# Performance work log

Measured on AMD Instinct MI355X. Metric: run time of the kernel, lower is better.

## Reference

```python
import jax, jax.numpy as jnp
import numpy as np

N_NODES = 30000
N_EDGES = 300000
NUM_GRAPHS = 512
HID = 600
IN_FEATS = 9
NUM_TASKS = 128


def setup_inputs() -> dict:
    key = jax.random.key(0)
    ks = jax.random.split(key, 20)
    s = 0.05  # small init scale to keep activations bounded over 5 layers
    inp = {
        'x': jax.random.normal(ks[0], (N_NODES, IN_FEATS), jnp.float32),
        'edge_index': jax.random.randint(ks[1], (2, N_EDGES), 0, N_NODES, jnp.int64),
        'batch_ind': jnp.sort(jax.random.randint(ks[2], (N_NODES,), 0, NUM_GRAPHS, jnp.int64)),
        'w1_0': jax.random.normal(ks[3], (IN_FEATS, HID), jnp.float32) * s,
        'b1_0': jax.random.normal(ks[4], (HID,), jnp.float32) * s,
        'w2_0': jax.random.normal(ks[5], (HID, HID), jnp.float32) * s,
        'b2_0': jax.random.normal(ks[6], (HID,), jnp.float32) * s,
        'w1_r': jax.random.normal(ks[7], (4, HID, HID), jnp.float32) * s,
        'b1_r': jax.random.normal(ks[8], (4, HID), jnp.float32) * s,
        'w2_r': jax.random.normal(ks[9], (4, HID, HID), jnp.float32) * s,
        'b2_r': jax.random.normal(ks[10], (4, HID), jnp.float32) * s,
        'cw1': jax.random.normal(ks[11], (HID, 256), jnp.float32) * s,
        'cb1': jax.random.normal(ks[12], (256,), jnp.float32) * s,
        'cw2': jax.random.normal(ks[13], (256, 256), jnp.float32) * s,
        'cb2': jax.random.normal(ks[14], (256,), jnp.float32) * s,
        'cw3': jax.random.normal(ks[15], (256, NUM_TASKS), jnp.float32) * s,
        'cb3': jax.random.normal(ks[16], (NUM_TASKS,), jnp.float32) * s,
    }
    return inp


def _gin_conv(h, edge_index, w1, b1, w2, b2):
    # sum-aggregate neighbor features: messages flow src -> dst
    msgs = h[edge_index[0]]                                   # [E, d] gather
    agg = jax.ops.segment_sum(msgs, edge_index[1], num_segments=N_NODES)
    z = h + agg                                               # (1 + eps) * x + agg, eps = 0
    z = jax.nn.relu(z @ w1 + b1) @ w2 + b2                    # per-layer MLP [in, 600, 600]
    return z


def _forward(x, edge_index, batch_ind, w1_0, b1_0, w2_0, b2_0,
             w1_r, b1_r, w2_r, b2_r, cw1, cb1, cw2, cb2, cw3, cb3):
    h = _gin_conv(x, edge_index, w1_0, b1_0, w2_0, b2_0)
    h = jax.nn.relu(h)  # inter-layer activation (dropout is identity in eval)
    for i in range(4):  # layers 1..4 (fixed, structurally distinct params)
        h = _gin_conv(h, edge_index, w1_r[i], b1_r[i], w2_r[i], b2_r[i])
        if i < 3:
            h = jax.nn.relu(h)  # no act/dropout after final GNN layer (jk=None)
    feats = jax.ops.segment_sum(h, batch_ind, num_segments=NUM_GRAPHS)  # global_add_pool
    z = jax.nn.relu(feats @ cw1 + cb1)
    z = jax.nn.relu(z @ cw2 + cb2)
    return z @ cw3 + cb3  # [NUM_GRAPHS, NUM_TASKS]


def reference(x, edge_index, batch_ind, w1_0, b1_0, w2_0, b2_0,
              w1_r, b1_r, w2_r, b2_r, cw1, cb1, cw2, cb2, cw3, cb3):
    return _forward(x, edge_index, batch_ind, w1_0, b1_0, w2_0, b2_0,
                    w1_r, b1_r, w2_r, b2_r, cw1, cb1, cw2, cb2, cw3, cb3)
```

## Files before the change

kernel.cpp:

```cpp
#include <hip/hip_runtime.h>

#define N_NODES 30000
#define N_EDGES 300000
#define NUM_GRAPHS 512
#define HID 600
#define IN_FEATS 9
#define NUM_TASKS 128

#define MPAD 30208
#define HPAD 640
#define K0PAD 32

typedef __attribute__((ext_vector_type(4))) float f32x4;
typedef __attribute__((ext_vector_type(8))) short bf16x8;


__device__ __forceinline__ float bflo(unsigned int v) {
  union { unsigned int u; float f; } c; c.u = v << 16; return c.f;
}
__device__ __forceinline__ float bfhi(unsigned int v) {
  union { unsigned int u; float f; } c; c.u = v & 0xffff0000u; return c.f;
}
__device__ __forceinline__ unsigned short f2bf(float f) {
  union { float f; unsigned int u; } c; c.f = f;
  unsigned int u = c.u;
  return (unsigned short)((u + 0x7fffu + ((u >> 16) & 1u)) >> 16);
}
__device__ __forceinline__ unsigned int pack2(float a, float b) {
  return (unsigned int)f2bf(a) | ((unsigned int)f2bf(b) << 16);
}


__global__ void k_setup(const float* __restrict__ w1_0,
                        const float* __restrict__ b1_0, const float* __restrict__ b2_0,
                        const float* __restrict__ b1_r, const float* __restrict__ b2_r,
                        const float* __restrict__ x,
                        const int* __restrict__ e_dst, const int* __restrict__ batch,
                        unsigned short* __restrict__ wt0, float* __restrict__ biases,
                        unsigned short* __restrict__ xb,
                        int* __restrict__ counts, int* __restrict__ gcnt) {
  const int S0 = HPAD * K0PAD;
  const int S1 = 10 * HPAD;
  const int S2 = MPAD * K0PAD;
  const int S3 = N_EDGES;
  int idx = blockIdx.x * 256 + threadIdx.x;
  if (idx < S0) {
    int n = idx / K0PAD, k = idx % K0PAD;
    float v = (n < HID && k < IN_FEATS) ? w1_0[(size_t)k * HID + n] : 0.f;
    wt0[idx] = f2bf(v);
    return;
  }
  idx -= S0;
  if (idx < S1) {
    int w = idx / HPAD, i = idx % HPAD;
    float v = 0.f;
    if (i < HID) {
      if (w == 0) v = b1_0[i];
      else if (w == 1) v = b2_0[i];
      else if (w < 6) v = b1_r[(size_t)(w - 2) * HID + i];
      else v = b2_r[(size_t)(w - 6) * HID + i];
    }
    biases[idx] = v;
    return;
  }
  idx -= S1;
  if (idx < S2) {
    int m = idx >> 5, k = idx & 31;
    float v = (m < N_NODES && k < IN_FEATS) ? x[(size_t)m * IN_FEATS + k] : 0.f;
    xb[idx] = f2bf(v);
    return;
  }
  idx -= S2;
  if (idx < S3) {
    atomicAdd(&counts[e_dst[idx]], 1);
    return;
  }
  idx -= S3;
  if (idx < N_NODES) {
    atomicAdd(&gcnt[batch[idx]], 1);
  }
}


__global__ __launch_bounds__(1024) void k_exscan(const int* __restrict__ in,
                                                 int* __restrict__ out,
                                                 int* cursor, int n) {
  __shared__ int buf[1024];
  int tid = threadIdx.x;
  int CH = (n + 1023) / 1024;
  int base = tid * CH;
  int s = 0;
  for (int j = 0; j < CH; ++j) {
    int i = base + j;
    if (i < n) s += in[i];
  }
  buf[tid] = s;
  __syncthreads();
  for (int off = 1; off < 1024; off <<= 1) {
    int t = (tid >= off) ? buf[tid - off] : 0;
    __syncthreads();
    buf[tid] += t;
    __syncthreads();
  }
  int pre = (tid == 0) ? 0 : buf[tid - 1];
  for (int j = 0; j < CH; ++j) {
    int i = base + j;
    if (i <= n) out[i] = pre;
    if (i < n) {
      int v = in[i];
      if (cursor) cursor[i] = pre;
      pre += v;
    }
  }
}

__global__ __launch_bounds__(256) void k_scan1(const int* __restrict__ in,
                                               int* __restrict__ partials, int n) {
  __shared__ int buf[256];
  int i = blockIdx.x * 256 + threadIdx.x;
  buf[threadIdx.x] = (i < n) ? in[i] : 0;
  __syncthreads();
  for (int off = 128; off; off >>= 1) {
    if (threadIdx.x < off) buf[threadIdx.x] += buf[threadIdx.x + off];
    __syncthreads();
  }
  if (threadIdx.x == 0) partials[blockIdx.x] = buf[0];
}

__global__ __launch_bounds__(256) void k_scan3(const int* __restrict__ in,
                                               const int* __restrict__ poff,
                                               int* __restrict__ out,
                                               int* __restrict__ cursor, int n) {
  __shared__ int buf[256];
  int b = blockIdx.x, t = threadIdx.x;
  int i = b * 256 + t;
  int v = (i < n) ? in[i] : 0;
  buf[t] = v;
  __syncthreads();
  for (int off = 1; off < 256; off <<= 1) {
    int x = (t >= off) ? buf[t - off] : 0;
    __syncthreads();
    buf[t] += x;
    __syncthreads();
  }
  int base = poff[b];
  int excl = base + buf[t] - v;
  if (i < n) {
    out[i] = excl;
    cursor[i] = excl;
    if (i == n - 1) out[n] = base + buf[t];
  }
}

__global__ void k_scatter(const int* __restrict__ src, const int* __restrict__ dst,
                          int* __restrict__ cursor, int* __restrict__ edge_src, int E) {
  int e = blockIdx.x * blockDim.x + threadIdx.x;
  if (e < E) {
    int pos = atomicAdd(&cursor[dst[e]], 1);
    edge_src[pos] = src[e];
  }
}


__global__ __launch_bounds__(256) void k_wt_tiled(
    const float* __restrict__ w2_0, const float* __restrict__ w1_r,
    const float* __restrict__ w2_r, unsigned short* __restrict__ wts) {
  __shared__ float tile[64][65];
  int b = blockIdx.x;
  int w = b / 100;
  int tb = b % 100;
  int tn = (tb % 10) * 64;
  int tk = (tb / 10) * 64;
  const float* W;
  if (w == 0) W = w2_0;
  else if (w < 5) W = w1_r + (size_t)(w - 1) * HID * HID;
  else W = w2_r + (size_t)(w - 5) * HID * HID;
  int t = threadIdx.x;
  int lx = t & 63, ly = t >> 6;
#pragma unroll
  for (int i = 0; i < 16; ++i) {
    int k = tk + ly + i * 4;
    int n = tn + lx;
    float v = (k < HID && n < HID) ? W[(size_t)k * HID + n] : 0.f;
    tile[ly + i * 4][lx] = v;
  }
  __syncthreads();
  unsigned short* dst = wts + (size_t)w * HPAD * HPAD;
#pragma unroll
  for (int i = 0; i < 16; ++i) {
    int n = tn + ly + i * 4;
    int k = tk + lx;
    dst[(size_t)n * HPAD + k] = f2bf(tile[lx][ly + i * 4]);
  }
}


template <int U>
__global__ __launch_bounds__(256) void k_agg_bf16(
    const unsigned int* __restrict__ h, const int* __restrict__ ptr,
    const int* __restrict__ esrc, unsigned int* __restrict__ z, int n_nodes) {
  int wave = threadIdx.x >> 6, lane = threadIdx.x & 63;
  int node = blockIdx.x * 4 + wave;
  if (node >= n_nodes) return;
  int beg = ptr[node], end = ptr[node + 1];
  const unsigned int* hn = h + (size_t)node * U;
  float a0[5], a1[5];
#pragma unroll
  for (int i = 0; i < 5; ++i) {
    int u = lane + i * 64;
    if (u < U) { unsigned int v = hn[u]; a0[i] = bflo(v); a1[i] = bfhi(v); }
    else { a0[i] = 0.f; a1[i] = 0.f; }
  }
  int e = beg;
  for (; e + 4 <= end; e += 4) {
    const unsigned int* p0 = h + (size_t)esrc[e] * U;
    const unsigned int* p1 = h + (size_t)esrc[e + 1] * U;
    const unsigned int* p2 = h + (size_t)esrc[e + 2] * U;
    const unsigned int* p3 = h + (size_t)esrc[e + 3] * U;
    unsigned int v0[5], v1[5], v2[5], v3[5];
#pragma unroll
    for (int i = 0; i < 5; ++i) {
      int u = lane + i * 64;
      if (u < U) { v0[i] = p0[u]; v1[i] = p1[u]; v2[i] = p2[u]; v3[i] = p3[u]; }
      else { v0[i] = 0; v1[i] = 0; v2[i] = 0; v3[i] = 0; }
    }
#pragma unroll
    for (int i = 0; i < 5; ++i) {
      a0[i] += (bflo(v0[i]) + bflo(v1[i])) + (bflo(v2[i]) + bflo(v3[i]));
      a1[i] += (bfhi(v0[i]) + bfhi(v1[i])) + (bfhi(v2[i]) + bfhi(v3[i]));
    }
  }
  for (; e < end; ++e) {
    const unsigned int* p0 = h + (size_t)esrc[e] * U;
#pragma unroll
    for (int i = 0; i < 5; ++i) {
      int u = lane + i * 64;
      if (u < U) { unsigned int v = p0[u]; a0[i] += bflo(v); a1[i] += bfhi(v); }
    }
  }
  unsigned int* zn = z + (size_t)node * U;
#pragma unroll
  for (int i = 0; i < 5; ++i) {
    int u = lane + i * 64;
    if (u < U) zn[u] = pack2(a0[i], a1[i]);
  }
}


#define GLOAD(gptr, lptr)                                                            \
  __builtin_amdgcn_global_load_lds(                                                  \
      (const __attribute__((address_space(1))) unsigned int*)(gptr),                 \
      (__attribute__((address_space(3))) unsigned int*)(lptr), 16, 0, 0)

template <int SWZ>
__global__ __launch_bounds__(512, 6) void k_mgemm_t(
    const unsigned short* __restrict__ A, const unsigned short* __restrict__ Bt,
    const float* __restrict__ bias, unsigned short* __restrict__ C,
    int lda, int ldb, int ldc, int K, int relu, int gy) {
  int G = gridDim.x;
  int orig = blockIdx.x;
  int q = G >> 3, r = G & 7;
  int xcd = orig & 7, local = orig >> 3;
  int wgid = (xcd < r ? xcd * (q + 1) : r * (q + 1) + (xcd - r) * q) + local;
  int n0 = (wgid % gy) * 128;
  int m0 = (wgid / gy) * 128;

  __shared__ unsigned short smem[3 * 4096 * 2];
  unsigned short* Asb = smem;
  unsigned short* Bsb = smem + 12288;

  int t = threadIdx.x;
  int lane = t & 63, wave = t >> 6;
  int wm = (wave >> 2) * 64;
  int wn = (wave & 3) * 32;

  f32x4 acc[4][2] = {};

  int off = t * 8;
  int rm = off >> 5, rk = off & 31;
  int rksrc = SWZ ? ((((rk >> 3) ^ (rm & 3)) & 3) << 3) : rk;

  const unsigned short* Ar = A + (size_t)(m0 + rm) * lda + rksrc;
  const unsigned short* Br = Bt + (size_t)(n0 + rm) * ldb + rksrc;

  int nt = K >> 5;
  GLOAD(Ar, Asb + off);
  GLOAD(Br, Bsb + off);
  if (nt > 1) {
    GLOAD(Ar + 32, Asb + 4096 + off);
    GLOAD(Br + 32, Bsb + 4096 + off);
  }

  int qq = lane >> 4;
  int ra = wm + (lane & 15);
  int rb = wn + (lane & 15);
  int kka = SWZ ? ((qq ^ (ra & 3)) << 3) : (qq << 3);
  int kkb = SWZ ? ((qq ^ (rb & 3)) << 3) : (qq << 3);
  int cur = 0;

  for (int tt = 0; tt < nt; ++tt) {
    if (tt + 1 < nt) {
      asm volatile("s_waitcnt vmcnt(2)" ::: "memory");
    } else {
      asm volatile("s_waitcnt vmcnt(0)" ::: "memory");
    }
    __builtin_amdgcn_s_barrier();
    if (tt + 2 < nt) {
      int k2 = (tt + 2) << 5;
      int nb = cur + 2; if (nb >= 3) nb -= 3;
      GLOAD(Ar + k2, Asb + nb * 4096 + off);
      GLOAD(Br + k2, Bsb + nb * 4096 + off);
    }
    bf16x8 a[4], b[2];
#pragma unroll
    for (int i = 0; i < 4; ++i)
      a[i] = *(const bf16x8*)(Asb + cur * 4096 + (ra + i * 16) * 32 + kka);
#pragma unroll
    for (int j = 0; j < 2; ++j)
      b[j] = *(const bf16x8*)(Bsb + cur * 4096 + (rb + j * 16) * 32 + kkb);
#pragma unroll
    for (int i = 0; i < 4; ++i)
#pragma unroll
      for (int j = 0; j < 2; ++j)
        acc[i][j] = __builtin_amdgcn_mfma_f32_16x16x32_bf16(b[j], a[i], acc[i][j], 0, 0, 0);
    cur += 1; if (cur >= 3) cur = 0;
  }

  __syncthreads();
  int colm = lane & 15;
  int nq = (lane >> 4) * 4;
#pragma unroll
  for (int j = 0; j < 2; ++j) {
    int nloc = wn + j * 16 + nq;
    f32x4 bv = *(const f32x4*)&bias[n0 + nloc];
#pragma unroll
    for (int i = 0; i < 4; ++i) {
      int mloc = wm + i * 16 + colm;
      float v0 = acc[i][j][0] + bv[0];
      float v1 = acc[i][j][1] + bv[1];
      float v2 = acc[i][j][2] + bv[2];
      float v3 = acc[i][j][3] + bv[3];
      if (relu) {
        v0 = fmaxf(v0, 0.f); v1 = fmaxf(v1, 0.f);
        v2 = fmaxf(v2, 0.f); v3 = fmaxf(v3, 0.f);
      }
      uint2 w;
      w.x = pack2(v0, v1);
      w.y = pack2(v2, v3);
      int nblk = (nloc >> 2) ^ ((mloc & 7) << 2);
      *(uint2*)&smem[mloc * 128 + nblk * 4] = w;
    }
  }
  __syncthreads();
#pragma unroll
  for (int p = 0; p < 4; ++p) {
    int idx = p * 4096 + t * 8;
    int mloc = idx >> 7;
    int ncol = idx & 127;
    int s = (mloc & 7) << 2;
    int nb0 = (ncol >> 2) ^ s;
    int nb1 = ((ncol >> 2) + 1) ^ s;
    uint2 w0 = *(uint2*)&smem[mloc * 128 + nb0 * 4];
    uint2 w1 = *(uint2*)&smem[mloc * 128 + nb1 * 4];
    uint4 w;
    w.x = w0.x; w.y = w0.y; w.z = w1.x; w.w = w1.y;
    *(uint4*)&C[(size_t)(m0 + mloc) * ldc + n0 + ncol] = w;
  }
}


__global__ __launch_bounds__(256) void k_poolcls(
    const unsigned int* __restrict__ h, const int* __restrict__ gptr,
    const float* __restrict__ cw1, const float* __restrict__ cb1,
    const float* __restrict__ cw2, const float* __restrict__ cb2,
    const float* __restrict__ cw3, const float* __restrict__ cb3,
    float* __restrict__ out) {
  const int U = HPAD / 2;
  __shared__ float red[4][HPAD];
  __shared__ float f[HPAD];
  __shared__ float red2[4][256];
  __shared__ float z1[256];
  __shared__ float z2[256];
  int g = blockIdx.x;
  int t = threadIdx.x;
  int wave = t >> 6, lane = t & 63;
  int beg = gptr[g], end = gptr[g + 1];

  {
    float a0[5] = {0.f, 0.f, 0.f, 0.f, 0.f}, a1[5] = {0.f, 0.f, 0.f, 0.f, 0.f};
    for (int i = beg + wave; i < end; i += 4) {
      const unsigned int* hi = h + (size_t)i * U;
#pragma unroll
      for (int j = 0; j < 5; ++j) {
        unsigned int v = hi[lane + j * 64];
        a0[j] += bflo(v); a1[j] += bfhi(v);
      }
    }
#pragma unroll
    for (int j = 0; j < 5; ++j) {
      int u = lane + j * 64;
      red[wave][2 * u] = a0[j];
      red[wave][2 * u + 1] = a1[j];
    }
  }
  __syncthreads();
  for (int c = t; c < HPAD; c += 256)
    f[c] = red[0][c] + red[1][c] + red[2][c] + red[3][c];
  __syncthreads();

  {
    float acc[4] = {0.f, 0.f, 0.f, 0.f};
    int k0 = wave * 150, k1 = k0 + 150;
    for (int k = k0; k < k1; ++k) {
      float fv = f[k];
      const float* row = cw1 + (size_t)k * 256;
#pragma unroll
      for (int j = 0; j < 4; ++j) acc[j] += fv * row[lane + j * 64];
    }
#pragma unroll
    for (int j = 0; j < 4; ++j) red2[wave][lane + j * 64] = acc[j];
  }
  __syncthreads();
  z1[t] = fmaxf(red2[0][t] + red2[1][t] + red2[2][t] + red2[3][t] + cb1[t], 0.f);
  __syncthreads();

  {
    float acc[4] = {0.f, 0.f, 0.f, 0.f};
    int k0 = wave * 64, k1 = k0 + 64;
    for (int k = k0; k < k1; ++k) {
      float zv = z1[k];
      const float* row = cw2 + (size_t)k * 256;
#pragma unroll
      for (int j = 0; j < 4; ++j) acc[j] += zv * row[lane + j * 64];
    }
    __syncthreads();
#pragma unroll
    for (int j = 0; j < 4; ++j) red2[wave][lane + j * 64] = acc[j];
  }
  __syncthreads();
  z2[t] = fmaxf(red2[0][t] + red2[1][t] + red2[2][t] + red2[3][t] + cb2[t], 0.f);
  __syncthreads();

  {
    float a0 = 0.f, a1 = 0.f;
    int k0 = wave * 64, k1 = k0 + 64;
    for (int k = k0; k < k1; ++k) {
      float zv = z2[k];
      const float* row = cw3 + (size_t)k * NUM_TASKS;
      a0 += zv * row[lane];
      a1 += zv * row[lane + 64];
    }
    __syncthreads();
    red2[wave][lane] = a0;
    red2[wave][lane + 64] = a1;
  }
  __syncthreads();
  if (t < NUM_TASKS)
    out[(size_t)g * NUM_TASKS + t] = red2[0][t] + red2[1][t] + red2[2][t] + red2[3][t] + cb3[t];
}


extern "C" void kernel_launch(void* const* d_in, const int* in_sizes, int n_in,
                              void* d_out, int out_size, void* d_ws, size_t ws_size,
                              hipStream_t stream) {
  const float* x      = (const float*)d_in[0];
  const int*   ei     = (const int*)d_in[1];
  const int*   batch  = (const int*)d_in[2];
  const float* w1_0   = (const float*)d_in[3];
  const float* b1_0   = (const float*)d_in[4];
  const float* w2_0   = (const float*)d_in[5];
  const float* b2_0   = (const float*)d_in[6];
  const float* w1_r   = (const float*)d_in[7];
  const float* b1_r   = (const float*)d_in[8];
  const float* w2_r   = (const float*)d_in[9];
  const float* b2_r   = (const float*)d_in[10];
  const float* cw1    = (const float*)d_in[11];
  const float* cb1    = (const float*)d_in[12];
  const float* cw2    = (const float*)d_in[13];
  const float* cb2    = (const float*)d_in[14];
  const float* cw3    = (const float*)d_in[15];
  const float* cb3    = (const float*)d_in[16];
  float* out = (float*)d_out;

  const int* e_src = ei;
  const int* e_dst = ei + N_EDGES;

  const size_t HBUF = (size_t)MPAD * HPAD;
  const size_t ZBUF = (size_t)MPAD * K0PAD;
  const size_t WT   = (size_t)HPAD * HPAD;
  const int NB = (N_NODES + 255) / 256;

  unsigned short* hA  = (unsigned short*)d_ws;
  unsigned short* hB  = hA + HBUF;
  unsigned short* hC  = hB + HBUF;
  unsigned short* z0  = hC + HBUF;
  unsigned short* xb  = z0 + ZBUF;
  unsigned short* wt0 = xb + ZBUF;
  unsigned short* wts = wt0 + (size_t)HPAD * K0PAD;
  float* biases = (float*)(wts + 9 * WT);
  int* row_ptr  = (int*)(biases + 10 * HPAD);
  int* counts   = row_ptr + (N_NODES + 1);
  int* edge_src = counts + N_NODES;
  int* gptr     = edge_src + N_EDGES;
  int* gcnt     = gptr + (NUM_GRAPHS + 1);
  int* partials = gcnt + NUM_GRAPHS;
  int* poff     = partials + (NB + 1);

  hipMemsetAsync(counts, 0, N_NODES * sizeof(int), stream);
  hipMemsetAsync(gcnt, 0, NUM_GRAPHS * sizeof(int), stream);
  {
    int total = HPAD * K0PAD + 10 * HPAD + MPAD * K0PAD + N_EDGES + N_NODES;
    k_setup<<<(total + 255) / 256, 256, 0, stream>>>(
        w1_0, b1_0, b2_0, b1_r, b2_r, x, e_dst, batch, wt0, biases, xb, counts, gcnt);
  }
  k_wt_tiled<<<9 * 100, 256, 0, stream>>>(w2_0, w1_r, w2_r, wts);

  k_scan1<<<NB, 256, 0, stream>>>(counts, partials, N_NODES);
  k_exscan<<<1, 1024, 0, stream>>>(partials, poff, nullptr, NB);
  k_scan3<<<NB, 256, 0, stream>>>(counts, poff, row_ptr, counts, N_NODES);
  k_scatter<<<(N_EDGES + 255) / 256, 256, 0, stream>>>(e_src, e_dst, counts, edge_src, N_EDGES);
  k_exscan<<<1, 1024, 0, stream>>>(gcnt, gptr, nullptr, NUM_GRAPHS);

  const int G16 = (MPAD / 128) * (HPAD / 128);
  const int GY = HPAD / 128;

  k_agg_bf16<K0PAD / 2><<<(N_NODES + 3) / 4, 256, 0, stream>>>(
      (const unsigned int*)xb, row_ptr, edge_src, (unsigned int*)z0, N_NODES);
  k_mgemm_t<0><<<G16, 512, 0, stream>>>(z0, wt0, biases + 0 * HPAD, hC, K0PAD, K0PAD, HPAD, K0PAD, 1, GY);
  k_mgemm_t<0><<<G16, 512, 0, stream>>>(hC, wts, biases + 1 * HPAD, hA, HPAD, HPAD, HPAD, HPAD, 1, GY);

  unsigned short* h = hA;
  unsigned short* z = hB;
  unsigned short* tb = hC;
  for (int i = 0; i < 4; ++i) {
    k_agg_bf16<HPAD / 2><<<(N_NODES + 3) / 4, 256, 0, stream>>>(
        (const unsigned int*)h, row_ptr, edge_src, (unsigned int*)z, N_NODES);
    if (i < 2) {
      k_mgemm_t<0><<<G16, 512, 0, stream>>>(z, wts + (1 + (size_t)i) * WT, biases + (2 + i) * HPAD, tb,
                                            HPAD, HPAD, HPAD, HPAD, 1, GY);
      k_mgemm_t<0><<<G16, 512, 0, stream>>>(tb, wts + (5 + (size_t)i) * WT, biases + (6 + i) * HPAD, z,
                                            HPAD, HPAD, HPAD, HPAD, 1, GY);
    } else {
      k_mgemm_t<1><<<G16, 512, 0, stream>>>(z, wts + (1 + (size_t)i) * WT, biases + (2 + i) * HPAD, tb,
                                            HPAD, HPAD, HPAD, HPAD, 1, GY);
      k_mgemm_t<1><<<G16, 512, 0, stream>>>(tb, wts + (5 + (size_t)i) * WT, biases + (6 + i) * HPAD, z,
                                            HPAD, HPAD, HPAD, HPAD, (i < 3) ? 1 : 0, GY);
    }
    unsigned short* tmp = h; h = z; z = tmp;
  }

  k_poolcls<<<NUM_GRAPHS, 256, 0, stream>>>((const unsigned int*)h, gptr,
                                            cw1, cb1, cw2, cb2, cw3, cb3, out);
}
```

Measured before the change: 709.9 us.

## Add full-width 128x640 GEMM tile kernel for last two GIN layers

Adds a wide GEMM kernel in which each block computes a 128-row by full 640-column output tile, so every A row-tile is loaded once and reused across all output columns. Each wave holds a 64x160 fp32 accumulator block, and the epilogue writes bf16 directly instead of staging through shared memory. The swizzled template variant is removed, and the plain kernel keeps the unswizzled path. Only the layer 3 and 4 MLP GEMMs use the wide kernel. The trade is much higher register and LDS use (launch bounds 512,2, three stages of 48KB), fewer blocks (236) and therefore lower occupancy, and uncoalesced 8-byte direct stores.

```diff
diff --git a/kernel.cpp b/kernel.cpp
--- a/kernel.cpp
+++ b/kernel.cpp
@@ -252,8 +252,7 @@
       (const __attribute__((address_space(1))) unsigned int*)(gptr),                 \
       (__attribute__((address_space(3))) unsigned int*)(lptr), 16, 0, 0)
 
-template <int SWZ>
-__global__ __launch_bounds__(512, 6) void k_mgemm_t(
+__global__ __launch_bounds__(512, 6) void k_mgemm(
     const unsigned short* __restrict__ A, const unsigned short* __restrict__ Bt,
     const float* __restrict__ bias, unsigned short* __restrict__ C,
     int lda, int ldb, int ldc, int K, int relu, int gy) {
@@ -278,10 +277,9 @@
 
   int off = t * 8;
   int rm = off >> 5, rk = off & 31;
-  int rksrc = SWZ ? ((((rk >> 3) ^ (rm & 3)) & 3) << 3) : rk;
-
-  const unsigned short* Ar = A + (size_t)(m0 + rm) * lda + rksrc;
-  const unsigned short* Br = Bt + (size_t)(n0 + rm) * ldb + rksrc;
+
+  const unsigned short* Ar = A + (size_t)(m0 + rm) * lda + rk;
+  const unsigned short* Br = Bt + (size_t)(n0 + rm) * ldb + rk;
 
   int nt = K >> 5;
   GLOAD(Ar, Asb + off);
@@ -291,11 +289,9 @@
     GLOAD(Br + 32, Bsb + 4096 + off);
   }
 
-  int qq = lane >> 4;
+  int kk = (lane >> 4) * 8;
   int ra = wm + (lane & 15);
   int rb = wn + (lane & 15);
-  int kka = SWZ ? ((qq ^ (ra & 3)) << 3) : (qq << 3);
-  int kkb = SWZ ? ((qq ^ (rb & 3)) << 3) : (qq << 3);
   int cur = 0;
 
   for (int tt = 0; tt < nt; ++tt) {
@@ -314,10 +310,10 @@
     bf16x8 a[4], b[2];
 #pragma unroll
     for (int i = 0; i < 4; ++i)
-      a[i] = *(const bf16x8*)(Asb + cur * 4096 + (ra + i * 16) * 32 + kka);
+      a[i] = *(const bf16x8*)(Asb + cur * 4096 + (ra + i * 16) * 32 + kk);
 #pragma unroll
     for (int j = 0; j < 2; ++j)
-      b[j] = *(const bf16x8*)(Bsb + cur * 4096 + (rb + j * 16) * 32 + kkb);
+      b[j] = *(const bf16x8*)(Bsb + cur * 4096 + (rb + j * 16) * 32 + kk);
 #pragma unroll
     for (int i = 0; i < 4; ++i)
 #pragma unroll
@@ -366,6 +362,106 @@
     w.x = w0.x; w.y = w0.y; w.z = w1.x; w.w = w1.y;
     *(uint4*)&C[(size_t)(m0 + mloc) * ldc + n0 + ncol] = w;
   }
+}
+
+
+__global__ __launch_bounds__(512, 2) void k_mgemm_wide(
+    const unsigned short* __restrict__ A, const unsigned short* __restrict__ Bt,
+    const float* __restrict__ bias, unsigned short* __restrict__ C,
+    int lda, int ldb, int ldc, int K, int relu) {
+  int m0 = blockIdx.x * 128;
+
+  __shared__ unsigned short smem[3 * 24576];
+  int t = threadIdx.x;
+  int lane = t & 63, wave = t >> 6;
+  int wm = (wave >> 2) * 64;
+  int wn = (wave & 3) * 160;
+
+  f32x4 acc[4][10] = {};
+
+  int rm = t >> 2, rk = (t & 3) * 8;
+  int rksrc = (((rk >> 3) ^ (rm & 3)) & 3) << 3;
+  const unsigned short* Ar = A + (size_t)(m0 + rm) * lda + rksrc;
+  const unsigned short* Br0 = Bt + (size_t)(rm) * ldb + rksrc;
+
+  int nt = K >> 5;
+
+#define WSTAGE(buf, koff)                                                  \
+  do {                                                                     \
+    GLOAD(Ar + (koff), smem + (buf) * 24576 + t * 8);                      \
+    _Pragma("unroll")                                                      \
+    for (int c = 0; c < 5; ++c)                                            \
+      GLOAD(Br0 + (size_t)(c) * 128 * ldb + (koff),                        \
+            smem + (buf) * 24576 + 4096 + c * 4096 + t * 8);               \
+  } while (0)
+
+  WSTAGE(0, 0);
+  if (nt > 1) WSTAGE(1, 32);
+
+  int qq = lane >> 4;
+  int ra = wm + (lane & 15);
+  int rb = wn + (lane & 15);
+  int kka = ((qq ^ (ra & 3)) & 3) << 3;
+  int kkb = ((qq ^ (rb & 3)) & 3) << 3;
+  int cur = 0;
+
+  for (int tt = 0; tt < nt; ++tt) {
+    if (tt + 1 < nt) {
+      asm volatile("s_waitcnt vmcnt(6)" ::: "memory");
+    } else {
+      asm volatile("s_waitcnt vmcnt(0)" ::: "memory");
+    }
+    __builtin_amdgcn_s_barrier();
+    if (tt + 2 < nt) {
+      int nb = cur + 2; if (nb >= 3) nb -= 3;
+      WSTAGE(nb, (tt + 2) << 5);
+    }
+    const unsigned short* Ab = smem + cur * 24576;
+    const unsigned short* Bb = smem + cur * 24576 + 4096;
+    bf16x8 a[4];
+#pragma unroll
+    for (int i = 0; i < 4; ++i)
+      a[i] = *(const bf16x8*)(Ab + (ra + i * 16) * 32 + kka);
+#pragma unroll
+    for (int jh = 0; jh < 2; ++jh) {
+      bf16x8 b[5];
+#pragma unroll
+      for (int jj = 0; jj < 5; ++jj)
+        b[jj] = *(const bf16x8*)(Bb + (rb + (jh * 5 + jj) * 16) * 32 + kkb);
+#pragma unroll
+      for (int i = 0; i < 4; ++i)
+#pragma unroll
+        for (int jj = 0; jj < 5; ++jj)
+          acc[i][jh * 5 + jj] =
+              __builtin_amdgcn_mfma_f32_16x16x32_bf16(b[jj], a[i], acc[i][jh * 5 + jj], 0, 0, 0);
+    }
+    cur += 1; if (cur >= 3) cur = 0;
+  }
+
+  int colm = lane & 15;
+  int nq4 = qq * 4;
+#pragma unroll
+  for (int j = 0; j < 10; ++j) {
+    int nloc = wn + j * 16 + nq4;
+    f32x4 bv = *(const f32x4*)&bias[nloc];
+#pragma unroll
+    for (int i = 0; i < 4; ++i) {
+      int m = m0 + wm + i * 16 + colm;
+      float v0 = acc[i][j][0] + bv[0];
+      float v1 = acc[i][j][1] + bv[1];
+      float v2 = acc[i][j][2] + bv[2];
+      float v3 = acc[i][j][3] + bv[3];
+      if (relu) {
+        v0 = fmaxf(v0, 0.f); v1 = fmaxf(v1, 0.f);
+        v2 = fmaxf(v2, 0.f); v3 = fmaxf(v3, 0.f);
+      }
+      uint2 w;
+      w.x = pack2(v0, v1);
+      w.y = pack2(v2, v3);
+      *(uint2*)&C[(size_t)m * ldc + nloc] = w;
+    }
+  }
+#undef WSTAGE
 }
 
 
@@ -522,12 +618,13 @@
   k_exscan<<<1, 1024, 0, stream>>>(gcnt, gptr, nullptr, NUM_GRAPHS);
 
   const int G16 = (MPAD / 128) * (HPAD / 128);
+  const int GW  = MPAD / 128;
   const int GY = HPAD / 128;
 
   k_agg_bf16<K0PAD / 2><<<(N_NODES + 3) / 4, 256, 0, stream>>>(
       (const unsigned int*)xb, row_ptr, edge_src, (unsigned int*)z0, N_NODES);
-  k_mgemm_t<0><<<G16, 512, 0, stream>>>(z0, wt0, biases + 0 * HPAD, hC, K0PAD, K0PAD, HPAD, K0PAD, 1, GY);
-  k_mgemm_t<0><<<G16, 512, 0, stream>>>(hC, wts, biases + 1 * HPAD, hA, HPAD, HPAD, HPAD, HPAD, 1, GY);
+  k_mgemm<<<G16, 512, 0, stream>>>(z0, wt0, biases + 0 * HPAD, hC, K0PAD, K0PAD, HPAD, K0PAD, 1, GY);
+  k_mgemm<<<G16, 512, 0, stream>>>(hC, wts, biases + 1 * HPAD, hA, HPAD, HPAD, HPAD, HPAD, 1, GY);
 
   unsigned short* h = hA;
   unsigned short* z = hB;
@@ -536,15 +633,15 @@
     k_agg_bf16<HPAD / 2><<<(N_NODES + 3) / 4, 256, 0, stream>>>(
         (const unsigned int*)h, row_ptr, edge_src, (unsigned int*)z, N_NODES);
     if (i < 2) {
-      k_mgemm_t<0><<<G16, 512, 0, stream>>>(z, wts + (1 + (size_t)i) * WT, biases + (2 + i) * HPAD, tb,
-                                            HPAD, HPAD, HPAD, HPAD, 1, GY);
-      k_mgemm_t<0><<<G16, 512, 0, stream>>>(tb, wts + (5 + (size_t)i) * WT, biases + (6 + i) * HPAD, z,
-                                            HPAD, HPAD, HPAD, HPAD, 1, GY);
+      k_mgemm<<<G16, 512, 0, stream>>>(z, wts + (1 + (size_t)i) * WT, biases + (2 + i) * HPAD, tb,
+                                       HPAD, HPAD, HPAD, HPAD, 1, GY);
+      k_mgemm<<<G16, 512, 0, stream>>>(tb, wts + (5 + (size_t)i) * WT, biases + (6 + i) * HPAD, z,
+                                       HPAD, HPAD, HPAD, HPAD, 1, GY);
     } else {
-      k_mgemm_t<1><<<G16, 512, 0, stream>>>(z, wts + (1 + (size_t)i) * WT, biases + (2 + i) * HPAD, tb,
-                                            HPAD, HPAD, HPAD, HPAD, 1, GY);
-      k_mgemm_t<1><<<G16, 512, 0, stream>>>(tb, wts + (5 + (size_t)i) * WT, biases + (6 + i) * HPAD, z,
-                                            HPAD, HPAD, HPAD, HPAD, (i < 3) ? 1 : 0, GY);
+      k_mgemm_wide<<<GW, 512, 0, stream>>>(z, wts + (1 + (size_t)i) * WT, biases + (2 + i) * HPAD, tb,
+                                           HPAD, HPAD, HPAD, HPAD, 1);
+      k_mgemm_wide<<<GW, 512, 0, stream>>>(tb, wts + (5 + (size_t)i) * WT, biases + (6 + i) * HPAD, z,
+                                           HPAD, HPAD, HPAD, HPAD, (i < 3) ? 1 : 0);
     }
     unsigned short* tmp = h; h = z; z = tmp;
   }
```

Result: no change. 716.3 us (+0.9%).
